# Performance work log

Hardware: AMD Instinct MI355X
Metric: run time of the kernel (lower is better)

The kernel has to match this reference:

```python
import jax, jax.numpy as jnp
import numpy as np

D_MODEL = 4096
N_EXPERTS = 64
TOP_K = 2
EPS = 1e-8


def setup_inputs() -> dict:
    key = jax.random.key(0)
    k1, k2, k3, k4 = jax.random.split(key, 4)
    hidden_states = jax.random.normal(k1, (4, 4096, D_MODEL), dtype=jnp.float32)
    routing_bias = jax.random.normal(k2, (4, N_EXPERTS), dtype=jnp.float32)
    # nn.Linear(d_model, n_experts): weight [n_experts, d_model], bias [n_experts]
    bound = 1.0 / np.sqrt(D_MODEL)
    W = jax.random.uniform(k3, (N_EXPERTS, D_MODEL), dtype=jnp.float32, minval=-bound, maxval=bound)
    b = jax.random.uniform(k4, (N_EXPERTS,), dtype=jnp.float32, minval=-bound, maxval=bound)
    return {"hidden_states": hidden_states, "routing_bias": routing_bias, "W": W, "b": b}


def reference(hidden_states, routing_bias, W, b):
    # router logits: [B, S, E]
    logits = jnp.einsum("bsd,ed->bse", hidden_states, W) + b
    logits = logits + routing_bias[:, None, :]
    expert_weights = jax.nn.softmax(logits, axis=-1)
    top_k_weights, top_k_indices = jax.lax.top_k(expert_weights, TOP_K)
    top_k_weights = top_k_weights / (jnp.sum(top_k_weights, axis=-1, keepdims=True) + EPS)
    return top_k_weights, top_k_indices
```

## Files before the change

kernel.cpp:

```cpp
#include <hip/hip_runtime.h>
#include <hip/hip_bf16.h>
#include <stdint.h>


#define D    4096
#define NE   64
#define TOKB 64
#define KQ   1024
#define NIT  (KQ / 32)

typedef __attribute__((ext_vector_type(8))) short bf16x8;
typedef __attribute__((ext_vector_type(4))) float f32x4;

__device__ __forceinline__ short f2bf(float x) {
    __hip_bfloat16 h = __float2bfloat16(x);
    return *reinterpret_cast<short*>(&h);
}
__device__ __forceinline__ float bf2f(short s) {
    unsigned int u = ((unsigned int)(unsigned short)s) << 16;
    return __uint_as_float(u);
}
__device__ __forceinline__ void split3(float x, short& s1, short& s2, short& s3) {
    short a = f2bf(x);  float r1 = x - bf2f(a);
    short b = f2bf(r1); float r2 = r1 - bf2f(b);
    s1 = a; s2 = b; s3 = f2bf(r2);
}

__global__ void wsplit3_kernel(const float* __restrict__ W,
                               short* __restrict__ W1, short* __restrict__ W2,
                               short* __restrict__ W3) {
    const int n = NE * D;
    for (int i = blockIdx.x * blockDim.x + threadIdx.x; i < n;
         i += gridDim.x * blockDim.x) {
        short a, b, c;
        split3(W[i], a, b, c);
        W1[i] = a; W2[i] = b; W3[i] = c;
    }
}

template<bool WPRE>
__global__ __launch_bounds__(512)
void router_mfma6(const float* __restrict__ hidden,
                  const float* __restrict__ rbias,
                  const float* __restrict__ W,
                  const float* __restrict__ bias,
                  const short* __restrict__ W1,
                  const short* __restrict__ W2,
                  const short* __restrict__ W3,
                  float* __restrict__ out)
{
    __shared__ float Lp[2][TOKB][NE + 2];

    const int tid  = threadIdx.x;
    const int lane = tid & 63;
    const int w    = tid >> 6;
    const int kq   = w >> 1;
    const int th   = w & 1;
    const int tokbase = blockIdx.x * TOKB;
    const int batch   = tokbase >> 12;

    const int r16 = lane & 15;
    const int kg  = (lane >> 4) * 8;

    const float* hA[2];
    hA[0] = hidden + (size_t)(tokbase + th * 32 + r16) * D + kq * KQ + kg;
    hA[1] = hA[0] + (size_t)16 * D;

    const short* w1p[4]; const short* w2p[4]; const short* w3p[4];
    const float* wfp[4];
    #pragma unroll
    for (int t = 0; t < 4; ++t) {
        const size_t off = (size_t)(16 * t + r16) * D + kq * KQ + kg;
        if (WPRE) { w1p[t] = W1 + off; w2p[t] = W2 + off; w3p[t] = W3 + off; }
        else      { wfp[t] = W + off; }
    }

    f32x4 aH[2][4], aL[2][4];
    #pragma unroll
    for (int tt = 0; tt < 2; ++tt)
        #pragma unroll
        for (int t = 0; t < 4; ++t) {
            aH[tt][t] = (f32x4){0.f, 0.f, 0.f, 0.f};
            aL[tt][t] = (f32x4){0.f, 0.f, 0.f, 0.f};
        }

    for (int it = 0; it < NIT; ++it) {
        bf16x8 h1[2], h2[2], h3[2];
        #pragma unroll
        for (int tt = 0; tt < 2; ++tt) {
            const float4 a0 = *(const float4*)(hA[tt]);
            const float4 a1 = *(const float4*)(hA[tt] + 4);
            hA[tt] += 32;
            const float av[8] = {a0.x, a0.y, a0.z, a0.w, a1.x, a1.y, a1.z, a1.w};
            #pragma unroll
            for (int e = 0; e < 8; ++e) {
                short s1, s2, s3;
                split3(av[e], s1, s2, s3);
                h1[tt][e] = s1; h2[tt][e] = s2; h3[tt][e] = s3;
            }
        }
        #pragma unroll
        for (int t = 0; t < 4; ++t) {
            bf16x8 x1, x2, x3;
            if constexpr (WPRE) {
                x1 = *(const bf16x8*)(w1p[t]);
                x2 = *(const bf16x8*)(w2p[t]);
                x3 = *(const bf16x8*)(w3p[t]);
                w1p[t] += 32; w2p[t] += 32; w3p[t] += 32;
            } else {
                const float4 b0 = *(const float4*)(wfp[t]);
                const float4 b1 = *(const float4*)(wfp[t] + 4);
                wfp[t] += 32;
                const float bv[8] = {b0.x, b0.y, b0.z, b0.w, b1.x, b1.y, b1.z, b1.w};
                #pragma unroll
                for (int e = 0; e < 8; ++e) {
                    short s1, s2, s3;
                    split3(bv[e], s1, s2, s3);
                    x1[e] = s1; x2[e] = s2; x3[e] = s3;
                }
            }
            #pragma unroll
            for (int tt = 0; tt < 2; ++tt) {
                aH[tt][t] = __builtin_amdgcn_mfma_f32_16x16x32_bf16(h1[tt], x1, aH[tt][t], 0, 0, 0);
                aL[tt][t] = __builtin_amdgcn_mfma_f32_16x16x32_bf16(h1[tt], x2, aL[tt][t], 0, 0, 0);
                aL[tt][t] = __builtin_amdgcn_mfma_f32_16x16x32_bf16(h2[tt], x1, aL[tt][t], 0, 0, 0);
                aL[tt][t] = __builtin_amdgcn_mfma_f32_16x16x32_bf16(h2[tt], x2, aL[tt][t], 0, 0, 0);
                aL[tt][t] = __builtin_amdgcn_mfma_f32_16x16x32_bf16(h1[tt], x3, aL[tt][t], 0, 0, 0);
                aL[tt][t] = __builtin_amdgcn_mfma_f32_16x16x32_bf16(h3[tt], x1, aL[tt][t], 0, 0, 0);
            }
        }
    }

    const int trow  = (lane >> 4) * 4;
    const int plane = kq & 1;
    float vals[2][4][4];
    #pragma unroll
    for (int tt = 0; tt < 2; ++tt)
        #pragma unroll
        for (int t = 0; t < 4; ++t)
            #pragma unroll
            for (int r = 0; r < 4; ++r)
                vals[tt][t][r] = aH[tt][t][r] + aL[tt][t][r];

    if (kq < 2) {
        #pragma unroll
        for (int tt = 0; tt < 2; ++tt)
            #pragma unroll
            for (int t = 0; t < 4; ++t)
                #pragma unroll
                for (int r = 0; r < 4; ++r)
                    Lp[plane][th * 32 + tt * 16 + trow + r][t * 16 + r16] = vals[tt][t][r];
    }
    __syncthreads();
    if (kq >= 2) {
        #pragma unroll
        for (int tt = 0; tt < 2; ++tt)
            #pragma unroll
            for (int t = 0; t < 4; ++t)
                #pragma unroll
                for (int r = 0; r < 4; ++r)
                    Lp[plane][th * 32 + tt * 16 + trow + r][t * 16 + r16] += vals[tt][t][r];
    }
    __syncthreads();

    if (tid < TOKB) {
        const int tok = tid;
        float m = -INFINITY, Z = 0.f;
        float v1 = -INFINITY, v2 = -INFINITY;
        int   i1 = 0, i2 = 0;
        for (int e = 0; e < NE; ++e) {
            const float dot = Lp[0][tok][e] + Lp[1][tok][e];
            const float v = (dot + bias[e]) + rbias[batch * NE + e];
            const float nm = fmaxf(m, v);
            Z = Z * __expf(m - nm) + __expf(v - nm);
            m = nm;
            const bool g1 = v > v1;
            const bool g2 = v > v2;
            const float nv2 = g1 ? v1 : (g2 ? v : v2);
            const int   ni2 = g1 ? i1 : (g2 ? e : i2);
            v1 = g1 ? v : v1;
            i1 = g1 ? e : i1;
            v2 = nv2;
            i2 = ni2;
        }
        const float p1 = __expf(v1 - m) / Z;
        const float p2 = __expf(v2 - m) / Z;
        const float s  = p1 + p2 + 1e-8f;
        const int gt = tokbase + tok;
        out[gt * 2 + 0] = p1 / s;
        out[gt * 2 + 1] = p2 / s;
        float* outI = out + 4 * 4096 * 2;
        outI[gt * 2 + 0] = (float)i1;
        outI[gt * 2 + 1] = (float)i2;
    }
}

extern "C" void kernel_launch(void* const* d_in, const int* in_sizes, int n_in,
                              void* d_out, int out_size, void* d_ws, size_t ws_size,
                              hipStream_t stream) {
    (void)in_sizes; (void)n_in; (void)out_size;
    const float* hidden = (const float*)d_in[0];
    const float* rbias  = (const float*)d_in[1];
    const float* W      = (const float*)d_in[2];
    const float* bias   = (const float*)d_in[3];
    float* out = (float*)d_out;

    const size_t wbytes = (size_t)3 * NE * D * sizeof(short);
    const bool wpre = (ws_size >= wbytes) && (d_ws != nullptr);
    short* W1 = (short*)d_ws;
    short* W2 = W1 + (size_t)NE * D;
    short* W3 = W2 + (size_t)NE * D;

    const int n_tokens = 4 * 4096;
    dim3 grid(n_tokens / TOKB);
    dim3 block(512);

    if (wpre) {
        hipLaunchKernelGGL(wsplit3_kernel, dim3(512), dim3(256), 0, stream, W, W1, W2, W3);
        hipLaunchKernelGGL((router_mfma6<true>), grid, block, 0, stream,
                           hidden, rbias, W, bias, W1, W2, W3, out);
    } else {
        hipLaunchKernelGGL((router_mfma6<false>), grid, block, 0, stream,
                           hidden, rbias, W, bias,
                           (const short*)nullptr, (const short*)nullptr,
                           (const short*)nullptr, out);
    }
}
```

Baseline: 461.5 us.

## Pre-swizzle weight fragments, double-buffer loads, and halve token tile per block

The weight split kernel now writes bf16 hi/mid/lo fragments in MFMA lane order, so each lane reads its B operands with contiguous coalesced 16-byte loads. The main loop is software-pipelined with two register buffers, issuing the next iteration's hidden and weight loads before computing the current one. Blocks shrink to 256 threads and 32 tokens each, with launch bounds allowing two blocks per CU, which doubles the grid. This costs more registers for the double buffers, and each weight fragment is now reused across half as many tokens.

```diff
diff --git a/kernel.cpp b/kernel.cpp
--- a/kernel.cpp
+++ b/kernel.cpp
@@ -3,11 +3,12 @@
 #include <stdint.h>
 
 
-#define D    4096
-#define NE   64
-#define TOKB 64
-#define KQ   1024
-#define NIT  (KQ / 32)
+#define D       4096
+#define NE      64
+#define TOKB    32
+#define KQ      1024
+#define NIT     (KQ / 32)
+#define WSTRIDE 6144
 
 typedef __attribute__((ext_vector_type(8))) short bf16x8;
 typedef __attribute__((ext_vector_type(4))) float f32x4;
@@ -20,60 +21,54 @@
     unsigned int u = ((unsigned int)(unsigned short)s) << 16;
     return __uint_as_float(u);
 }
-__device__ __forceinline__ void split3(float x, short& s1, short& s2, short& s3) {
-    short a = f2bf(x);  float r1 = x - bf2f(a);
-    short b = f2bf(r1); float r2 = r1 - bf2f(b);
-    s1 = a; s2 = b; s3 = f2bf(r2);
-}
-
-__global__ void wsplit3_kernel(const float* __restrict__ W,
-                               short* __restrict__ W1, short* __restrict__ W2,
-                               short* __restrict__ W3) {
-    const int n = NE * D;
-    for (int i = blockIdx.x * blockDim.x + threadIdx.x; i < n;
-         i += gridDim.x * blockDim.x) {
+__device__ __forceinline__ void split3(float x, short& a, short& b, short& c) {
+    a = f2bf(x);  float r  = x - bf2f(a);
+    b = f2bf(r);  float r2 = r - bf2f(b);
+    c = f2bf(r2);
+}
+
+__global__ void wfrag_kernel(const float* __restrict__ W, short* __restrict__ Wf) {
+    const int idx = blockIdx.x * blockDim.x + threadIdx.x;
+    if (idx >= 128 * 4 * 64) return;
+    const int l = idx & 63, t = (idx >> 6) & 3, s = idx >> 8;
+    const int e  = 16 * t + (l & 15);
+    const int kb = s * 32 + ((l >> 4) * 8);
+    bf16x8 c1, c2, c3;
+    #pragma unroll
+    for (int j = 0; j < 8; ++j) {
         short a, b, c;
-        split3(W[i], a, b, c);
-        W1[i] = a; W2[i] = b; W3[i] = c;
-    }
+        split3(W[(size_t)e * D + kb + j], a, b, c);
+        c1[j] = a; c2[j] = b; c3[j] = c;
+    }
+    *(bf16x8*)(Wf + ((size_t)((s * 3 + 0) * 4 + t) * 64 + l) * 8) = c1;
+    *(bf16x8*)(Wf + ((size_t)((s * 3 + 1) * 4 + t) * 64 + l) * 8) = c2;
+    *(bf16x8*)(Wf + ((size_t)((s * 3 + 2) * 4 + t) * 64 + l) * 8) = c3;
 }
 
 template<bool WPRE>
-__global__ __launch_bounds__(512)
-void router_mfma6(const float* __restrict__ hidden,
-                  const float* __restrict__ rbias,
-                  const float* __restrict__ W,
-                  const float* __restrict__ bias,
-                  const short* __restrict__ W1,
-                  const short* __restrict__ W2,
-                  const short* __restrict__ W3,
-                  float* __restrict__ out)
+__global__ __launch_bounds__(256, 2)
+void router5(const float* __restrict__ hidden,
+             const float* __restrict__ rbias,
+             const float* __restrict__ W,
+             const float* __restrict__ bias,
+             const short* __restrict__ Wf,
+             float* __restrict__ out)
 {
     __shared__ float Lp[2][TOKB][NE + 2];
 
     const int tid  = threadIdx.x;
     const int lane = tid & 63;
-    const int w    = tid >> 6;
-    const int kq   = w >> 1;
-    const int th   = w & 1;
+    const int kq   = tid >> 6;
     const int tokbase = blockIdx.x * TOKB;
     const int batch   = tokbase >> 12;
 
     const int r16 = lane & 15;
     const int kg  = (lane >> 4) * 8;
 
-    const float* hA[2];
-    hA[0] = hidden + (size_t)(tokbase + th * 32 + r16) * D + kq * KQ + kg;
-    hA[1] = hA[0] + (size_t)16 * D;
-
-    const short* w1p[4]; const short* w2p[4]; const short* w3p[4];
-    const float* wfp[4];
-    #pragma unroll
-    for (int t = 0; t < 4; ++t) {
-        const size_t off = (size_t)(16 * t + r16) * D + kq * KQ + kg;
-        if (WPRE) { w1p[t] = W1 + off; w2p[t] = W2 + off; w3p[t] = W3 + off; }
-        else      { wfp[t] = W + off; }
-    }
+    const float* h0 = hidden + (size_t)(tokbase + r16) * D + kq * KQ + kg;
+    const float* h1 = h0 + (size_t)16 * D;
+    const short* wv = Wf + (size_t)kq * NIT * WSTRIDE + lane * 8;
+    const float* wf0 = W + (size_t)r16 * D + kq * KQ + kg;
 
     f32x4 aH[2][4], aL[2][4];
     #pragma unroll
@@ -84,51 +79,62 @@
             aL[tt][t] = (f32x4){0.f, 0.f, 0.f, 0.f};
         }
 
-    for (int it = 0; it < NIT; ++it) {
-        bf16x8 h1[2], h2[2], h3[2];
-        #pragma unroll
-        for (int tt = 0; tt < 2; ++tt) {
-            const float4 a0 = *(const float4*)(hA[tt]);
-            const float4 a1 = *(const float4*)(hA[tt] + 4);
-            hA[tt] += 32;
-            const float av[8] = {a0.x, a0.y, a0.z, a0.w, a1.x, a1.y, a1.z, a1.w};
-            #pragma unroll
-            for (int e = 0; e < 8; ++e) {
-                short s1, s2, s3;
-                split3(av[e], s1, s2, s3);
-                h1[tt][e] = s1; h2[tt][e] = s2; h3[tt][e] = s3;
-            }
-        }
-        #pragma unroll
-        for (int t = 0; t < 4; ++t) {
-            bf16x8 x1, x2, x3;
-            if constexpr (WPRE) {
-                x1 = *(const bf16x8*)(w1p[t]);
-                x2 = *(const bf16x8*)(w2p[t]);
-                x3 = *(const bf16x8*)(w3p[t]);
-                w1p[t] += 32; w2p[t] += 32; w3p[t] += 32;
-            } else {
-                const float4 b0 = *(const float4*)(wfp[t]);
-                const float4 b1 = *(const float4*)(wfp[t] + 4);
-                wfp[t] += 32;
-                const float bv[8] = {b0.x, b0.y, b0.z, b0.w, b1.x, b1.y, b1.z, b1.w};
-                #pragma unroll
-                for (int e = 0; e < 8; ++e) {
-                    short s1, s2, s3;
-                    split3(bv[e], s1, s2, s3);
-                    x1[e] = s1; x2[e] = s2; x3[e] = s3;
-                }
-            }
-            #pragma unroll
-            for (int tt = 0; tt < 2; ++tt) {
-                aH[tt][t] = __builtin_amdgcn_mfma_f32_16x16x32_bf16(h1[tt], x1, aH[tt][t], 0, 0, 0);
-                aL[tt][t] = __builtin_amdgcn_mfma_f32_16x16x32_bf16(h1[tt], x2, aL[tt][t], 0, 0, 0);
-                aL[tt][t] = __builtin_amdgcn_mfma_f32_16x16x32_bf16(h2[tt], x1, aL[tt][t], 0, 0, 0);
-                aL[tt][t] = __builtin_amdgcn_mfma_f32_16x16x32_bf16(h2[tt], x2, aL[tt][t], 0, 0, 0);
-                aL[tt][t] = __builtin_amdgcn_mfma_f32_16x16x32_bf16(h1[tt], x3, aL[tt][t], 0, 0, 0);
-                aL[tt][t] = __builtin_amdgcn_mfma_f32_16x16x32_bf16(h3[tt], x1, aL[tt][t], 0, 0, 0);
-            }
-        }
+    bf16x8 WA[12], WB[12];
+    float4 HA[4], HB[4];
+
+    #define LOADH(HH, IT) do { \
+        const int itc = (IT) < NIT ? (IT) : NIT - 1; \
+        const float* p0 = h0 + itc * 32; \
+        const float* p1 = h1 + itc * 32; \
+        HH[0] = *(const float4*)p0; HH[1] = *(const float4*)(p0 + 4); \
+        HH[2] = *(const float4*)p1; HH[3] = *(const float4*)(p1 + 4); } while (0)
+
+    #define LOADW(WW, IT) do { \
+        const int itc = (IT) < NIT ? (IT) : NIT - 1; \
+        const short* wp = wv + (size_t)itc * WSTRIDE; \
+        _Pragma("unroll") \
+        for (int j = 0; j < 12; ++j) WW[j] = *(const bf16x8*)(wp + j * 512); } while (0)
+
+    #define COMPUTE(WW, HH, IT) do { \
+        bf16x8 b1[2], b2[2], b3[2]; \
+        _Pragma("unroll") \
+        for (int tt = 0; tt < 2; ++tt) { \
+            const float4 a0 = HH[tt * 2], a1 = HH[tt * 2 + 1]; \
+            const float av[8] = {a0.x, a0.y, a0.z, a0.w, a1.x, a1.y, a1.z, a1.w}; \
+            _Pragma("unroll") \
+            for (int e2 = 0; e2 < 8; ++e2) { \
+                short sa, sb, sc; split3(av[e2], sa, sb, sc); \
+                b1[tt][e2] = sa; b2[tt][e2] = sb; b3[tt][e2] = sc; } } \
+        _Pragma("unroll") \
+        for (int t = 0; t < 4; ++t) { \
+            bf16x8 x1, x2, x3; \
+            if constexpr (WPRE) { x1 = WW[0 * 4 + t]; x2 = WW[1 * 4 + t]; x3 = WW[2 * 4 + t]; } \
+            else { \
+                const float* wp = wf0 + (size_t)t * 16 * D + (IT) * 32; \
+                const float4 q0 = *(const float4*)wp, q1 = *(const float4*)(wp + 4); \
+                const float bv[8] = {q0.x, q0.y, q0.z, q0.w, q1.x, q1.y, q1.z, q1.w}; \
+                _Pragma("unroll") \
+                for (int e2 = 0; e2 < 8; ++e2) { \
+                    short sa, sb, sc; split3(bv[e2], sa, sb, sc); \
+                    x1[e2] = sa; x2[e2] = sb; x3[e2] = sc; } } \
+            _Pragma("unroll") \
+            for (int tt = 0; tt < 2; ++tt) { \
+                aH[tt][t] = __builtin_amdgcn_mfma_f32_16x16x32_bf16(b1[tt], x1, aH[tt][t], 0, 0, 0); \
+                aL[tt][t] = __builtin_amdgcn_mfma_f32_16x16x32_bf16(b1[tt], x2, aL[tt][t], 0, 0, 0); \
+                aL[tt][t] = __builtin_amdgcn_mfma_f32_16x16x32_bf16(b2[tt], x1, aL[tt][t], 0, 0, 0); \
+                aL[tt][t] = __builtin_amdgcn_mfma_f32_16x16x32_bf16(b2[tt], x2, aL[tt][t], 0, 0, 0); \
+                aL[tt][t] = __builtin_amdgcn_mfma_f32_16x16x32_bf16(b1[tt], x3, aL[tt][t], 0, 0, 0); \
+                aL[tt][t] = __builtin_amdgcn_mfma_f32_16x16x32_bf16(b3[tt], x1, aL[tt][t], 0, 0, 0); } } } while (0)
+
+    if constexpr (WPRE) LOADW(WA, 0);
+    LOADH(HA, 0);
+    for (int it = 0; it < NIT; it += 2) {
+        if constexpr (WPRE) LOADW(WB, it + 1);
+        LOADH(HB, it + 1);
+        COMPUTE(WA, HA, it);
+        if constexpr (WPRE) LOADW(WA, it + 2);
+        LOADH(HA, it + 2);
+        COMPUTE(WB, HB, it + 1);
     }
 
     const int trow  = (lane >> 4) * 4;
@@ -149,7 +155,7 @@
             for (int t = 0; t < 4; ++t)
                 #pragma unroll
                 for (int r = 0; r < 4; ++r)
-                    Lp[plane][th * 32 + tt * 16 + trow + r][t * 16 + r16] = vals[tt][t][r];
+                    Lp[plane][tt * 16 + trow + r][t * 16 + r16] = vals[tt][t][r];
     }
     __syncthreads();
     if (kq >= 2) {
@@ -159,7 +165,7 @@
             for (int t = 0; t < 4; ++t)
                 #pragma unroll
                 for (int r = 0; r < 4; ++r)
-                    Lp[plane][th * 32 + tt * 16 + trow + r][t * 16 + r16] += vals[tt][t][r];
+                    Lp[plane][tt * 16 + trow + r][t * 16 + r16] += vals[tt][t][r];
     }
     __syncthreads();
 
@@ -193,6 +199,9 @@
         outI[gt * 2 + 0] = (float)i1;
         outI[gt * 2 + 1] = (float)i2;
     }
+    #undef LOADH
+    #undef LOADW
+    #undef COMPUTE
 }
 
 extern "C" void kernel_launch(void* const* d_in, const int* in_sizes, int n_in,
@@ -207,22 +216,18 @@
 
     const size_t wbytes = (size_t)3 * NE * D * sizeof(short);
     const bool wpre = (ws_size >= wbytes) && (d_ws != nullptr);
-    short* W1 = (short*)d_ws;
-    short* W2 = W1 + (size_t)NE * D;
-    short* W3 = W2 + (size_t)NE * D;
+    short* Wf = (short*)d_ws;
 
     const int n_tokens = 4 * 4096;
     dim3 grid(n_tokens / TOKB);
-    dim3 block(512);
+    dim3 block(256);
 
     if (wpre) {
-        hipLaunchKernelGGL(wsplit3_kernel, dim3(512), dim3(256), 0, stream, W, W1, W2, W3);
-        hipLaunchKernelGGL((router_mfma6<true>), grid, block, 0, stream,
-                           hidden, rbias, W, bias, W1, W2, W3, out);
+        hipLaunchKernelGGL(wfrag_kernel, dim3(128), dim3(256), 0, stream, W, Wf);
+        hipLaunchKernelGGL((router5<true>), grid, block, 0, stream,
+                           hidden, rbias, W, bias, Wf, out);
     } else {
-        hipLaunchKernelGGL((router_mfma6<false>), grid, block, 0, stream,
-                           hidden, rbias, W, bias,
-                           (const short*)nullptr, (const short*)nullptr,
-                           (const short*)nullptr, out);
-    }
-}
+        hipLaunchKernelGGL((router5<false>), grid, block, 0, stream,
+                           hidden, rbias, W, bias, (const short*)nullptr, out);
+    }
+}
```

Result: no change. 456.2 us (-1.2%).
